# Kernel optimization log

Hardware: AMD Instinct MI355X
Metric: run time of the kernel (lower is better)

Reference implementation:

```python
import jax, jax.numpy as jnp
import numpy as np

B, D_IN, FD = 32768, 2048, 128
N1 = N2 = N3 = 4
T = 1.0  # temperature buffer value (eval mode)
LN_EPS = 1e-5

def _gelu(x):
    return jax.nn.gelu(x, approximate=False)  # torch nn.GELU default = exact erf

def setup_inputs() -> dict:
    key = jax.random.key(0)
    ks = iter(jax.random.split(key, 64))
    def rn(shape, s=0.02):
        return jax.random.normal(next(ks), shape, jnp.float32) * s
    inp = {"x": jax.random.normal(next(ks), (B, D_IN), jnp.float32)}
    # input_proj: Linear(2048,512) GELU Linear(512,256) LayerNorm(256)
    inp.update(ipW1=rn((D_IN, 512)), ipb1=jnp.zeros(512), ipW2=rn((512, 256)), ipb2=jnp.zeros(256),
               ln_g=jnp.ones(256), ln_b=jnp.zeros(256))
    def level(din, nc, pfx):
        return {pfx+"W3d": rn((din, 3)), pfx+"b3d": jnp.zeros(3),
                pfx+"c": rn((nc, 3), 0.3), pfx+"lr": jnp.zeros(nc),
                pfx+"f1W": rn((din, FD)), pfx+"f1b": jnp.zeros(FD),
                pfx+"f2W": rn((FD, FD)), pfx+"f2b": jnp.zeros(FD),
                pfx+"rW": rn((FD+3, nc)), pfx+"rb": jnp.zeros(nc)}
    inp.update(level(256, N1, "l1"))
    inp.update(level(FD, N2, "l2"))
    inp.update(level(FD, N3, "l3"))
    # expert_head: Linear(128+4+4+4, 256) GELU Linear(256, 64)
    inp.update(ehW1=rn((FD+N1+N2+N3, 256)), ehb1=jnp.zeros(256),
               ehW2=rn((256, N1*N2*N3)), ehb2=jnp.zeros(N1*N2*N3))
    return inp

def _level_fwd(x, W3d, b3d, c, f1W, f1b, f2W, f2b, rW, rb):
    # x: (B, din) -> probs (B, nc), features (B, FD)
    pos = x @ W3d + b3d                                   # (B, 3)
    d_sq = ((pos[:, None, :] - c[None, :, :]) ** 2).sum(-1)  # (B, nc)
    geo = -d_sq / (2.0 * T * T + 1e-8)                    # non-spectral geo signal
    feat = _gelu(x @ f1W + f1b) @ f2W + f2b               # (B, FD)
    logits = jnp.concatenate([feat, pos], axis=-1) @ rW + rb + 0.5 * geo
    probs = jax.nn.softmax(logits / max(T, 0.1), axis=-1)  # eval path: plain softmax
    return probs, feat

def _router_fwd(x, ipW1, ipb1, ipW2, ipb2, ln_g, ln_b,
                l1W3d, l1b3d, l1c, l1f1W, l1f1b, l1f2W, l1f2b, l1rW, l1rb,
                l2W3d, l2b3d, l2c, l2f1W, l2f1b, l2f2W, l2f2b, l2rW, l2rb,
                l3W3d, l3b3d, l3c, l3f1W, l3f1b, l3f2W, l3f2b, l3rW, l3rb,
                ehW1, ehb1, ehW2, ehb2):
    h = _gelu(x @ ipW1 + ipb1) @ ipW2 + ipb2
    mu = h.mean(-1, keepdims=True)
    var = ((h - mu) ** 2).mean(-1, keepdims=True)
    h = (h - mu) * jax.lax.rsqrt(var + LN_EPS) * ln_g + ln_b  # LayerNorm(256)
    p1, f1 = _level_fwd(h,  l1W3d, l1b3d, l1c, l1f1W, l1f1b, l1f2W, l1f2b, l1rW, l1rb)
    p2, f2 = _level_fwd(f1, l2W3d, l2b3d, l2c, l2f1W, l2f1b, l2f2W, l2f2b, l2rW, l2rb)
    p3, f3 = _level_fwd(f2, l3W3d, l3b3d, l3c, l3f1W, l3f1b, l3f2W, l3f2b, l3rW, l3rb)
    combined = jnp.concatenate([f3, p1, p2, p3], axis=-1)  # (B, 140)
    logits = _gelu(combined @ ehW1 + ehb1) @ ehW2 + ehb2   # (B, 64)
    expert_probs = jax.nn.softmax(logits / max(T, 0.1), axis=-1)
    return expert_probs

def reference(x, ipW1, ipb1, ipW2, ipb2, ln_g, ln_b,
              l1W3d, l1b3d, l1c, l1lr, l1f1W, l1f1b, l1f2W, l1f2b, l1rW, l1rb,
              l2W3d, l2b3d, l2c, l2lr, l2f1W, l2f1b, l2f2W, l2f2b, l2rW, l2rb,
              l3W3d, l3b3d, l3c, l3lr, l3f1W, l3f1b, l3f2W, l3f2b, l3rW, l3rb,
              ehW1, ehb1, ehW2, ehb2):
    # l?lr (log_radii) are unused in non-spectral mode, matching the source.
    expert_probs = _router_fwd(x, ipW1, ipb1, ipW2, ipb2, ln_g, ln_b,
                               l1W3d, l1b3d, l1c, l1f1W, l1f1b, l1f2W, l1f2b, l1rW, l1rb,
                               l2W3d, l2b3d, l2c, l2f1W, l2f1b, l2f2W, l2f2b, l2rW, l2rb,
                               l3W3d, l3b3d, l3c, l3f1W, l3f1b, l3f2W, l3f2b, l3rW, l3rb,
                               ehW1, ehb1, ehW2, ehb2)
    expert_ids = jnp.argmax(expert_probs, axis=-1)
    return expert_probs, expert_ids
```

## Files before the change

kernel.cpp:

```cpp
#include <hip/hip_runtime.h>
#include <hip/hip_bf16.h>
#include <cstdint>
#include <cstddef>


typedef short  s8v  __attribute__((ext_vector_type(8)));
typedef float  f4v  __attribute__((ext_vector_type(4)));
typedef float  f16v __attribute__((ext_vector_type(16)));
typedef unsigned int u32;

#define B_ROWS 32768

__device__ inline short f2bf(float x) {
    __hip_bfloat16 h = __float2bfloat16(x);
    return __builtin_bit_cast(short, h);
}
__device__ inline float bf2f(short s) {
    return __bfloat162float(__builtin_bit_cast(__hip_bfloat16, s));
}
__device__ inline float gelu_f(float x) {
    return 0.5f * x * (1.0f + erff(x * 0.70710678118654752440f));
}
__device__ inline void gload_lds16(const short* g, short* l) {
    __builtin_amdgcn_global_load_lds(
        (const __attribute__((address_space(1))) u32*)g,
        (__attribute__((address_space(3))) u32*)l, 16, 0, 0);
}

struct SplitDesc { const float* W; short* dst; int K, N, Kpad, blk0; };
struct SplitPack { SplitDesc d[10]; };

__global__ void split_all(SplitPack p) {
    const int bid = blockIdx.x;
    int i = 0;
    #pragma unroll
    for (int j = 1; j < 10; ++j) if (bid >= p.d[j].blk0) i = j;
    const SplitDesc& D = p.d[i];
    const int idx = (bid - D.blk0) * 256 + threadIdx.x;
    const int total = D.N * D.Kpad;
    if (idx >= total) return;
    const int n = idx / D.Kpad, k = idx - n * D.Kpad;
    const float v = (k < D.K) ? D.W[(size_t)k * D.N + n] : 0.0f;
    const short hs = f2bf(v);
    D.dst[idx] = hs;
    D.dst[total + idx] = f2bf(v - bf2f(hs));
}

template<int BM, int BN, int EPI>
__launch_bounds__(256, 2)
__global__ void gemm32(const float* __restrict__ A, int lda,
                       const short* __restrict__ Bsp, int ldb, int NK,
                       const float* __restrict__ bias, int K, int N, int ntiles,
                       float* __restrict__ out, float* __restrict__ out2)
{
    constexpr int MF  = BM / 64;
    constexpr int NFw = BN / 64;
    constexpr int BUF = (BM + BN) * 64;
    constexpr int FPT = BM / 8;
    constexpr int TPR = 32 / FPT;
    constexpr int nBI = BN / 32;
    __shared__ short smem[2 * BUF];

    const int tid = threadIdx.x;
    const int l   = tid & 63, wid = tid >> 6;
    const int wr  = wid >> 1, wc = wid & 1;
    const int bid = blockIdx.x;
    const int ntb = bid % ntiles, mtb = bid / ntiles;
    const int m0  = mtb * BM, n0 = ntb * BN;

    const int ar = tid / TPR, aseg = tid % TPR;
    const float* aP = A + (size_t)(m0 + ar) * lda + aseg * FPT;

    const short* bg[nBI];
    {
        const int cs = (l & 7) ^ (l >> 3);
        const int plane = cs >> 2, kslot = cs & 3;
        #pragma unroll
        for (int j = 0; j < nBI; ++j) {
            const int col = (wid * nBI + j) * 8 + (l >> 3);
            bg[j] = Bsp + (size_t)plane * NK + (size_t)(n0 + col) * ldb + kslot * 8;
        }
    }

    f16v acc[MF][NFw];
    #pragma unroll
    for (int m = 0; m < MF; ++m)
        #pragma unroll
        for (int n = 0; n < NFw; ++n) acc[m][n] = (f16v)0.0f;

    f4v areg[FPT / 4];

    auto loadA = [&](int t) {
        const float* p = aP + t * 32;
        #pragma unroll
        for (int i = 0; i < FPT / 4; ++i) areg[i] = *(const f4v*)(p + i * 4);
    };
    auto stageB = [&](int t, short* buf) {
        short* Bb = buf + BM * 64;
        #pragma unroll
        for (int j = 0; j < nBI; ++j)
            gload_lds16(bg[j] + t * 32, Bb + (wid * nBI + j) * 512);
    };
    auto writeA = [&](short* buf) {
        #pragma unroll
        for (int c = 0; c < FPT / 8; ++c) {
            s8v hi, lo;
            #pragma unroll
            for (int e = 0; e < 8; ++e) {
                const float v = areg[c * 2 + (e >> 2)][e & 3];
                const short hs = f2bf(v);
                hi[e] = hs; lo[e] = f2bf(v - bf2f(hs));
            }
            const int csh = aseg * (FPT / 8) + c;
            *(s8v*)&buf[ar * 64 + ((csh    ) ^ (ar & 7)) * 8] = hi;
            *(s8v*)&buf[ar * 64 + ((csh + 4) ^ (ar & 7)) * 8] = lo;
        }
    };
    auto compute = [&](const short* buf) {
        const short* Ab = buf;
        const short* Bb = buf + BM * 64;
        #pragma unroll
        for (int ks = 0; ks < 2; ++ks) {
            const int csb = ks * 2 + (l >> 5);
            s8v ah[MF], al[MF], bh[NFw], bl[NFw];
            #pragma unroll
            for (int m = 0; m < MF; ++m) {
                const int row = wr * (BM / 2) + m * 32 + (l & 31);
                ah[m] = *(const s8v*)&Ab[row * 64 + ((csb    ) ^ (row & 7)) * 8];
                al[m] = *(const s8v*)&Ab[row * 64 + ((csb + 4) ^ (row & 7)) * 8];
            }
            #pragma unroll
            for (int n = 0; n < NFw; ++n) {
                const int col = wc * (BN / 2) + n * 32 + (l & 31);
                bh[n] = *(const s8v*)&Bb[col * 64 + ((csb    ) ^ (col & 7)) * 8];
                bl[n] = *(const s8v*)&Bb[col * 64 + ((csb + 4) ^ (col & 7)) * 8];
            }
            __builtin_amdgcn_s_setprio(1);
            #pragma unroll
            for (int m = 0; m < MF; ++m)
                #pragma unroll
                for (int n = 0; n < NFw; ++n) {
                    acc[m][n] = __builtin_amdgcn_mfma_f32_32x32x16_bf16(ah[m], bh[n], acc[m][n], 0, 0, 0);
                    acc[m][n] = __builtin_amdgcn_mfma_f32_32x32x16_bf16(ah[m], bl[n], acc[m][n], 0, 0, 0);
                    acc[m][n] = __builtin_amdgcn_mfma_f32_32x32x16_bf16(al[m], bh[n], acc[m][n], 0, 0, 0);
                }
            __builtin_amdgcn_s_setprio(0);
        }
    };

    const int NT = K / 32;
    loadA(0);
    stageB(0, smem);
    writeA(smem);
    __syncthreads();
    for (int t = 0; t < NT; ++t) {
        short* curb = smem + (t & 1) * BUF;
        short* nxtb = smem + ((t & 1) ^ 1) * BUF;
        const bool pf = (t + 1 < NT);
        if (pf) { loadA(t + 1); stageB(t + 1, nxtb); }
        compute(curb);
        if (pf) writeA(nxtb);
        __syncthreads();
    }

    if constexpr (EPI <= 1) {
        #pragma unroll
        for (int m = 0; m < MF; ++m) {
            #pragma unroll
            for (int n = 0; n < NFw; ++n) {
                const int gcol = n0 + wc * (BN / 2) + n * 32 + (l & 31);
                const float bv = bias[gcol];
                #pragma unroll
                for (int r = 0; r < 16; ++r) {
                    const int grow = m0 + wr * (BM / 2) + m * 32
                                   + (r & 3) + 8 * (r >> 2) + 4 * (l >> 5);
                    float xv = acc[m][n][r] + bv;
                    if constexpr (EPI == 0) xv = gelu_f(xv);
                    out[(size_t)grow * N + gcol] = xv;
                }
            }
        }
    } else {
        float* LT = reinterpret_cast<float*>(smem);
        const int gcolL = wc * 32 + (l & 31);
        const float bv = bias[gcolL];
        #pragma unroll
        for (int r = 0; r < 16; ++r) {
            const int row = wr * 32 + (r & 3) + 8 * (r >> 2) + 4 * (l >> 5);
            LT[row * 64 + gcolL] = acc[0][0][r] + bv;
        }
        __syncthreads();
        const int r = tid >> 2, q = tid & 3;
        const float* Lr = LT + r * 64 + q * 16;
        float mx = Lr[0];
        #pragma unroll
        for (int c = 1; c < 16; ++c) mx = fmaxf(mx, Lr[c]);
        mx = fmaxf(mx, __shfl_xor(mx, 1));
        mx = fmaxf(mx, __shfl_xor(mx, 2));
        float ev[16]; float s = 0.0f;
        #pragma unroll
        for (int c = 0; c < 16; ++c) { ev[c] = expf(Lr[c] - mx); s += ev[c]; }
        s += __shfl_xor(s, 1);
        s += __shfl_xor(s, 2);
        float pmax = -1.0f; int arg = 0;
        #pragma unroll
        for (int c = 0; c < 16; ++c) {
            const float pv = ev[c] / s;
            out[(size_t)(m0 + r) * 64 + q * 16 + c] = pv;
            if (pv > pmax) { pmax = pv; arg = q * 16 + c; }
        }
        #pragma unroll
        for (int off = 1; off <= 2; off <<= 1) {
            const float po = __shfl_xor(pmax, off);
            const int   ao = __shfl_xor(arg, off);
            if (po > pmax || (po == pmax && ao < arg)) { pmax = po; arg = ao; }
        }
        if (q == 0) out2[m0 + r] = (float)arg;
    }
}

__global__ __launch_bounds__(256) void ln_kernel(float* __restrict__ H,
                                                 const float* __restrict__ G,
                                                 const float* __restrict__ Bv)
{
    const int row = blockIdx.x * 4 + (threadIdx.x >> 6);
    const int l   = threadIdx.x & 63;
    float* hr = H + (size_t)row * 256;
    f4v v = *reinterpret_cast<const f4v*>(&hr[l * 4]);
    float s = v[0] + v[1] + v[2] + v[3];
    #pragma unroll
    for (int o = 32; o; o >>= 1) s += __shfl_xor(s, o);
    const float mu = s * 0.00390625f;
    f4v d = v - mu;
    float q = d[0]*d[0] + d[1]*d[1] + d[2]*d[2] + d[3]*d[3];
    #pragma unroll
    for (int o = 32; o; o >>= 1) q += __shfl_xor(q, o);
    const float var = q * 0.00390625f;
    const float sc  = 1.0f / sqrtf(var + 1e-5f);
    f4v gg = *reinterpret_cast<const f4v*>(&G[l * 4]);
    f4v bb = *reinterpret_cast<const f4v*>(&Bv[l * 4]);
    f4v o4 = d * sc * gg + bb;
    *reinterpret_cast<f4v*>(&hr[l * 4]) = o4;
}

__global__ __launch_bounds__(256) void p_kernel(
    const float* __restrict__ X, int din,
    const float* __restrict__ F,
    const float* __restrict__ W3d, const float* __restrict__ b3d,
    const float* __restrict__ cc,
    const float* __restrict__ rW, const float* __restrict__ rb,
    float* __restrict__ P)
{
    const int row = blockIdx.x * 4 + (threadIdx.x >> 6);
    const int l   = threadIdx.x & 63;
    float px0 = 0.f, px1 = 0.f, px2 = 0.f;
    const int per = din >> 6;
    const float* xr = X + (size_t)row * din;
    for (int i = 0; i < per; ++i) {
        const int k = l + (i << 6);
        const float xv = xr[k];
        px0 += xv * W3d[k*3 + 0];
        px1 += xv * W3d[k*3 + 1];
        px2 += xv * W3d[k*3 + 2];
    }
    float g0 = 0.f, g1 = 0.f, g2 = 0.f, g3 = 0.f;
    const float* fr = F + (size_t)row * 128;
    #pragma unroll
    for (int i = 0; i < 2; ++i) {
        const int k = l + (i << 6);
        const float fv = fr[k];
        g0 += fv * rW[k*4 + 0]; g1 += fv * rW[k*4 + 1];
        g2 += fv * rW[k*4 + 2]; g3 += fv * rW[k*4 + 3];
    }
    #pragma unroll
    for (int o = 32; o; o >>= 1) {
        px0 += __shfl_xor(px0, o); px1 += __shfl_xor(px1, o); px2 += __shfl_xor(px2, o);
        g0  += __shfl_xor(g0, o);  g1  += __shfl_xor(g1, o);
        g2  += __shfl_xor(g2, o);  g3  += __shfl_xor(g3, o);
    }
    if (l == 0) {
        const float pos0 = px0 + b3d[0], pos1 = px1 + b3d[1], pos2 = px2 + b3d[2];
        float lg[4];
        float mx = -1e30f;
        float gg[4] = {g0, g1, g2, g3};
        #pragma unroll
        for (int c = 0; c < 4; ++c) {
            float a = gg[c] + rb[c]
                    + pos0 * rW[512 + c] + pos1 * rW[516 + c] + pos2 * rW[520 + c];
            const float d0 = pos0 - cc[c*3 + 0];
            const float d1 = pos1 - cc[c*3 + 1];
            const float d2 = pos2 - cc[c*3 + 2];
            a += 0.5f * (-(d0*d0 + d1*d1 + d2*d2) / 2.00000001f);
            lg[c] = a;
            mx = fmaxf(mx, a);
        }
        const float e0 = expf(lg[0]-mx), e1 = expf(lg[1]-mx),
                    e2 = expf(lg[2]-mx), e3 = expf(lg[3]-mx);
        const float s = e0 + e1 + e2 + e3;
        float* pr = P + (size_t)row * 4;
        pr[0] = e0/s; pr[1] = e1/s; pr[2] = e2/s; pr[3] = e3/s;
    }
}

__global__ void concat_kernel(const float* __restrict__ f3,
                              const float* __restrict__ P1,
                              const float* __restrict__ P2,
                              const float* __restrict__ P3,
                              float* __restrict__ C)
{
    const int idx = blockIdx.x * 256 + threadIdx.x;
    const int row = idx / 160, j = idx - row * 160;
    float v;
    if      (j < 128) v = f3[(size_t)row * 128 + j];
    else if (j < 132) v = P1[(size_t)row * 4 + (j - 128)];
    else if (j < 136) v = P2[(size_t)row * 4 + (j - 132)];
    else if (j < 140) v = P3[(size_t)row * 4 + (j - 136)];
    else              v = 0.0f;
    C[idx] = v;
}

extern "C" void kernel_launch(void* const* d_in, const int* in_sizes, int n_in,
                              void* d_out, int out_size, void* d_ws, size_t ws_size,
                              hipStream_t stream)
{
    (void)in_sizes; (void)n_in; (void)out_size; (void)ws_size;

    const float* x    = (const float*)d_in[0];
    const float* ipW1 = (const float*)d_in[1];
    const float* ipb1 = (const float*)d_in[2];
    const float* ipW2 = (const float*)d_in[3];
    const float* ipb2 = (const float*)d_in[4];
    const float* ln_g = (const float*)d_in[5];
    const float* ln_b = (const float*)d_in[6];
    const float* W3d[3] = {(const float*)d_in[7],  (const float*)d_in[17], (const float*)d_in[27]};
    const float* b3d[3] = {(const float*)d_in[8],  (const float*)d_in[18], (const float*)d_in[28]};
    const float* cc[3]  = {(const float*)d_in[9],  (const float*)d_in[19], (const float*)d_in[29]};
    const float* f1W[3] = {(const float*)d_in[11], (const float*)d_in[21], (const float*)d_in[31]};
    const float* f1b[3] = {(const float*)d_in[12], (const float*)d_in[22], (const float*)d_in[32]};
    const float* f2W[3] = {(const float*)d_in[13], (const float*)d_in[23], (const float*)d_in[33]};
    const float* f2b[3] = {(const float*)d_in[14], (const float*)d_in[24], (const float*)d_in[34]};
    const float* rW[3]  = {(const float*)d_in[15], (const float*)d_in[25], (const float*)d_in[35]};
    const float* rb[3]  = {(const float*)d_in[16], (const float*)d_in[26], (const float*)d_in[36]};
    const float* ehW1 = (const float*)d_in[37];
    const float* ehb1 = (const float*)d_in[38];
    const float* ehW2 = (const float*)d_in[39];
    const float* ehb2 = (const float*)d_in[40];

    size_t off = 0;
    auto take = [&](size_t bytes) -> void* {
        void* p = (char*)d_ws + off;
        off += (bytes + 255) & ~(size_t)255;
        return p;
    };
    auto takeW = [&](int N, int Kpad) -> short* {
        return (short*)take((size_t)2 * N * Kpad * 2);
    };
    short* W1s = takeW(512, 2048);
    short* W2s = takeW(256, 512);
    short* L1a = takeW(128, 256);
    short* L1b = takeW(128, 128);
    short* L2a = takeW(128, 128);
    short* L2b = takeW(128, 128);
    short* L3a = takeW(128, 128);
    short* L3b = takeW(128, 128);
    short* E1s = takeW(256, 160);
    short* E2s = takeW(64, 256);
    float* h1 = (float*)take((size_t)B_ROWS * 512 * 4);
    float* h2 = (float*)take((size_t)B_ROWS * 256 * 4);
    float* zg = (float*)take((size_t)B_ROWS * 128 * 4);
    float* f1 = (float*)take((size_t)B_ROWS * 128 * 4);
    float* f2 = (float*)take((size_t)B_ROWS * 128 * 4);
    float* f3 = (float*)take((size_t)B_ROWS * 128 * 4);
    float* p1 = (float*)take((size_t)B_ROWS * 4 * 4);
    float* p2 = (float*)take((size_t)B_ROWS * 4 * 4);
    float* p3 = (float*)take((size_t)B_ROWS * 4 * 4);
    float* comb = h1;
    float* geh  = (float*)((char*)h1 + ((size_t)22 << 20));

    SplitPack sp;
    int blk = 0;
    auto desc = [&](int i, const float* W, short* dst, int K, int N, int Kpad) {
        sp.d[i] = {W, dst, K, N, Kpad, blk};
        blk += (N * Kpad + 255) / 256;
    };
    desc(0, ipW1,   W1s, 2048, 512, 2048);
    desc(1, ipW2,   W2s,  512, 256,  512);
    desc(2, f1W[0], L1a,  256, 128,  256);
    desc(3, f2W[0], L1b,  128, 128,  128);
    desc(4, f1W[1], L2a,  128, 128,  128);
    desc(5, f2W[1], L2b,  128, 128,  128);
    desc(6, f1W[2], L3a,  128, 128,  128);
    desc(7, f2W[2], L3b,  128, 128,  128);
    desc(8, ehW1,   E1s,  140, 256,  160);
    desc(9, ehW2,   E2s,  256,  64,  256);
    split_all<<<blk, 256, 0, stream>>>(sp);

    const dim3 blkT(256);
    constexpr int MG128 = B_ROWS / 128;
    constexpr int MG64  = B_ROWS / 64;

    gemm32<128,128,0><<<MG128*4, blkT, 0, stream>>>(x,  2048, W1s, 2048, 512*2048, ipb1, 2048, 512, 4, h1, nullptr);
    gemm32<128,128,1><<<MG128*2, blkT, 0, stream>>>(h1,  512, W2s,  512, 256*512,  ipb2,  512, 256, 2, h2, nullptr);
    ln_kernel<<<B_ROWS/4, 256, 0, stream>>>(h2, ln_g, ln_b);

    gemm32<64,128,0><<<MG64, blkT, 0, stream>>>(h2, 256, L1a, 256, 128*256, f1b[0], 256, 128, 1, zg, nullptr);
    gemm32<64,128,1><<<MG64, blkT, 0, stream>>>(zg, 128, L1b, 128, 128*128, f2b[0], 128, 128, 1, f1, nullptr);
    p_kernel<<<B_ROWS/4, 256, 0, stream>>>(h2, 256, f1, W3d[0], b3d[0], cc[0], rW[0], rb[0], p1);

    gemm32<64,128,0><<<MG64, blkT, 0, stream>>>(f1, 128, L2a, 128, 128*128, f1b[1], 128, 128, 1, zg, nullptr);
    gemm32<64,128,1><<<MG64, blkT, 0, stream>>>(zg, 128, L2b, 128, 128*128, f2b[1], 128, 128, 1, f2, nullptr);
    p_kernel<<<B_ROWS/4, 256, 0, stream>>>(f1, 128, f2, W3d[1], b3d[1], cc[1], rW[1], rb[1], p2);

    gemm32<64,128,0><<<MG64, blkT, 0, stream>>>(f2, 128, L3a, 128, 128*128, f1b[2], 128, 128, 1, zg, nullptr);
    gemm32<64,128,1><<<MG64, blkT, 0, stream>>>(zg, 128, L3b, 128, 128*128, f2b[2], 128, 128, 1, f3, nullptr);
    p_kernel<<<B_ROWS/4, 256, 0, stream>>>(f2, 128, f3, W3d[2], b3d[2], cc[2], rW[2], rb[2], p3);

    concat_kernel<<<(B_ROWS*160)/256, 256, 0, stream>>>(f3, p1, p2, p3, comb);
    gemm32<64,128,0><<<MG64*2, blkT, 0, stream>>>(comb, 160, E1s, 160, 256*160, ehb1, 160, 256, 2, geh, nullptr);
    gemm32<64,64,2><<<MG64, blkT, 0, stream>>>(geh, 256, E2s, 256, 64*256, ehb2, 256, 64, 1,
                                               (float*)d_out, (float*)d_out + (size_t)B_ROWS * 64);
}
```

Baseline: 533.2 us.

## Add specialized first-layer GEMM with pre-swizzled split-bf16 weight image

Replaces the generic gemm32 for the 2048->512 input projection with a dedicated kernel. It reads the fp32 activations directly and splits them into bf16 hi/lo planes in registers. The weights are pre-split into a swizzled tile image that can be loaded straight into LDS with global_load_lds, and the block-to-tile mapping is XCD-aware. Single-stage LDS with register prefetch of the next A tile aims to cut conversion and layout overhead, but adds a new weight-prep kernel and a fixed-shape path that only fits these dimensions.

```diff
diff --git a/kernel.cpp b/kernel.cpp
--- a/kernel.cpp
+++ b/kernel.cpp
@@ -27,14 +27,150 @@
         (__attribute__((address_space(3))) u32*)l, 16, 0, 0);
 }
 
+__global__ void split_w1_img(const float* __restrict__ W, short* __restrict__ img)
+{
+    const int idx = blockIdx.x * 256 + threadIdx.x;
+    const int p = idx & 7;
+    const int n = (idx >> 3) & 511;
+    const int t = idx >> 12;
+    const int cs = p ^ (n & 7);
+    const int plane = cs >> 2, kc = cs & 3;
+    const int kbase = t * 32 + kc * 8;
+    s8v v8;
+    #pragma unroll
+    for (int e = 0; e < 8; ++e) {
+        const float v = W[(size_t)(kbase + e) * 512 + n];
+        const short h = f2bf(v);
+        v8[e] = plane ? f2bf(v - bf2f(h)) : h;
+    }
+    *(s8v*)&img[(size_t)((t * 512 + n) * 64 + p * 8)] = v8;
+}
+
+__launch_bounds__(256, 4)
+__global__ void gemm1k(const float* __restrict__ X,
+                       const short* __restrict__ Bimg,
+                       const float* __restrict__ bias,
+                       float* __restrict__ out)
+{
+    __shared__ short smem[128 * 64 * 2];
+    short* Ab = smem;
+    short* Bb = smem + 128 * 64;
+
+    const int tid = threadIdx.x;
+    const int l = tid & 63, wid = tid >> 6;
+    const int wr = wid >> 1, wc = wid & 1;
+
+    const int d = blockIdx.x;
+    const int xcd = d & 7;
+    const int m0 = ((xcd & 1) * 128 + (d >> 3)) * 128;
+    const int n0 = (xcd >> 1) * 128;
+
+    const int ar = tid & 127, ah = tid >> 7;
+    const float* xP = X + (size_t)(m0 + ar) * 2048 + ah * 16;
+    short* awr = Ab + ar * 64;
+    const int pw0 = ((ah * 2    ) ^ (ar & 7)) * 8;
+    const int pw1 = ((ah * 2 + 1) ^ (ar & 7)) * 8;
+    const int pw2 = ((ah * 2 + 4) ^ (ar & 7)) * 8;
+    const int pw3 = ((ah * 2 + 5) ^ (ar & 7)) * 8;
+
+    const short* bP = Bimg + (size_t)n0 * 64 + (size_t)(wid * 4) * 512 + (size_t)l * 8;
+    short* bD = Bb + wid * 4 * 512;
+
+    f16v acc[2][2];
+    #pragma unroll
+    for (int m = 0; m < 2; ++m)
+        #pragma unroll
+        for (int n = 0; n < 2; ++n) acc[m][n] = (f16v)0.0f;
+
+    f4v cur0, cur1, cur2, cur3;
+    cur0 = *(const f4v*)(xP + 0);
+    cur1 = *(const f4v*)(xP + 4);
+    cur2 = *(const f4v*)(xP + 8);
+    cur3 = *(const f4v*)(xP + 12);
+
+    for (int t = 0; t < 64; ++t) {
+        s8v hi0, hi1, lo0, lo1;
+        #pragma unroll
+        for (int e = 0; e < 4; ++e) {
+            float v;
+            short h;
+            v = cur0[e]; h = f2bf(v); hi0[e]     = h; lo0[e]     = f2bf(v - bf2f(h));
+            v = cur1[e]; h = f2bf(v); hi0[e + 4] = h; lo0[e + 4] = f2bf(v - bf2f(h));
+            v = cur2[e]; h = f2bf(v); hi1[e]     = h; lo1[e]     = f2bf(v - bf2f(h));
+            v = cur3[e]; h = f2bf(v); hi1[e + 4] = h; lo1[e + 4] = f2bf(v - bf2f(h));
+        }
+        __syncthreads();
+        *(s8v*)&awr[pw0] = hi0;
+        *(s8v*)&awr[pw1] = hi1;
+        *(s8v*)&awr[pw2] = lo0;
+        *(s8v*)&awr[pw3] = lo1;
+        {
+            const short* bt = bP + (size_t)t * 32768;
+            gload_lds16(bt,          bD);
+            gload_lds16(bt +  512,   bD + 512);
+            gload_lds16(bt + 1024,   bD + 1024);
+            gload_lds16(bt + 1536,   bD + 1536);
+        }
+        if (t < 63) {
+            const float* p = xP + (t + 1) * 32;
+            cur0 = *(const f4v*)(p + 0);
+            cur1 = *(const f4v*)(p + 4);
+            cur2 = *(const f4v*)(p + 8);
+            cur3 = *(const f4v*)(p + 12);
+        }
+        __syncthreads();
+
+        #pragma unroll
+        for (int ks = 0; ks < 2; ++ks) {
+            const int ph = (ks * 2 + (l >> 5)) ^ (l & 7);
+            s8v ahf[2], alf[2], bhf[2], blf[2];
+            #pragma unroll
+            for (int m = 0; m < 2; ++m) {
+                const int row = wr * 64 + m * 32 + (l & 31);
+                ahf[m] = *(const s8v*)&Ab[row * 64 + ph * 8];
+                alf[m] = *(const s8v*)&Ab[row * 64 + (ph ^ 4) * 8];
+            }
+            #pragma unroll
+            for (int n = 0; n < 2; ++n) {
+                const int col = wc * 64 + n * 32 + (l & 31);
+                bhf[n] = *(const s8v*)&Bb[col * 64 + ph * 8];
+                blf[n] = *(const s8v*)&Bb[col * 64 + (ph ^ 4) * 8];
+            }
+            #pragma unroll
+            for (int m = 0; m < 2; ++m)
+                #pragma unroll
+                for (int n = 0; n < 2; ++n) {
+                    acc[m][n] = __builtin_amdgcn_mfma_f32_32x32x16_bf16(ahf[m], bhf[n], acc[m][n], 0, 0, 0);
+                    acc[m][n] = __builtin_amdgcn_mfma_f32_32x32x16_bf16(ahf[m], blf[n], acc[m][n], 0, 0, 0);
+                    acc[m][n] = __builtin_amdgcn_mfma_f32_32x32x16_bf16(alf[m], bhf[n], acc[m][n], 0, 0, 0);
+                }
+        }
+    }
+
+    #pragma unroll
+    for (int m = 0; m < 2; ++m) {
+        #pragma unroll
+        for (int n = 0; n < 2; ++n) {
+            const int gcol = n0 + wc * 64 + n * 32 + (l & 31);
+            const float bv = bias[gcol];
+            #pragma unroll
+            for (int r = 0; r < 16; ++r) {
+                const int grow = m0 + wr * 64 + m * 32
+                               + (r & 3) + 8 * (r >> 2) + 4 * (l >> 5);
+                out[(size_t)grow * 512 + gcol] = gelu_f(acc[m][n][r] + bv);
+            }
+        }
+    }
+}
+
 struct SplitDesc { const float* W; short* dst; int K, N, Kpad, blk0; };
-struct SplitPack { SplitDesc d[10]; };
+struct SplitPack { SplitDesc d[9]; };
 
 __global__ void split_all(SplitPack p) {
     const int bid = blockIdx.x;
     int i = 0;
     #pragma unroll
-    for (int j = 1; j < 10; ++j) if (bid >= p.d[j].blk0) i = j;
+    for (int j = 1; j < 9; ++j) if (bid >= p.d[j].blk0) i = j;
     const SplitDesc& D = p.d[i];
     const int idx = (bid - D.blk0) * 256 + threadIdx.x;
     const int total = D.N * D.Kpad;
@@ -355,7 +491,7 @@
     auto takeW = [&](int N, int Kpad) -> short* {
         return (short*)take((size_t)2 * N * Kpad * 2);
     };
-    short* W1s = takeW(512, 2048);
+    short* W1img = (short*)take((size_t)64 * 512 * 64 * 2);
     short* W2s = takeW(256, 512);
     short* L1a = takeW(128, 256);
     short* L1b = takeW(128, 128);
@@ -377,29 +513,29 @@
     float* comb = h1;
     float* geh  = (float*)((char*)h1 + ((size_t)22 << 20));
 
+    split_w1_img<<<(64 * 512 * 8) / 256, 256, 0, stream>>>(ipW1, W1img);
     SplitPack sp;
     int blk = 0;
     auto desc = [&](int i, const float* W, short* dst, int K, int N, int Kpad) {
         sp.d[i] = {W, dst, K, N, Kpad, blk};
         blk += (N * Kpad + 255) / 256;
     };
-    desc(0, ipW1,   W1s, 2048, 512, 2048);
-    desc(1, ipW2,   W2s,  512, 256,  512);
-    desc(2, f1W[0], L1a,  256, 128,  256);
-    desc(3, f2W[0], L1b,  128, 128,  128);
-    desc(4, f1W[1], L2a,  128, 128,  128);
-    desc(5, f2W[1], L2b,  128, 128,  128);
-    desc(6, f1W[2], L3a,  128, 128,  128);
-    desc(7, f2W[2], L3b,  128, 128,  128);
-    desc(8, ehW1,   E1s,  140, 256,  160);
-    desc(9, ehW2,   E2s,  256,  64,  256);
+    desc(0, ipW2,   W2s,  512, 256,  512);
+    desc(1, f1W[0], L1a,  256, 128,  256);
+    desc(2, f2W[0], L1b,  128, 128,  128);
+    desc(3, f1W[1], L2a,  128, 128,  128);
+    desc(4, f2W[1], L2b,  128, 128,  128);
+    desc(5, f1W[2], L3a,  128, 128,  128);
+    desc(6, f2W[2], L3b,  128, 128,  128);
+    desc(7, ehW1,   E1s,  140, 256,  160);
+    desc(8, ehW2,   E2s,  256,  64,  256);
     split_all<<<blk, 256, 0, stream>>>(sp);
 
     const dim3 blkT(256);
     constexpr int MG128 = B_ROWS / 128;
     constexpr int MG64  = B_ROWS / 64;
 
-    gemm32<128,128,0><<<MG128*4, blkT, 0, stream>>>(x,  2048, W1s, 2048, 512*2048, ipb1, 2048, 512, 4, h1, nullptr);
+    gemm1k<<<1024, blkT, 0, stream>>>(x, W1img, ipb1, h1);
     gemm32<128,128,1><<<MG128*2, blkT, 0, stream>>>(h1,  512, W2s,  512, 256*512,  ipb2,  512, 256, 2, h2, nullptr);
     ln_kernel<<<B_ROWS/4, 256, 0, stream>>>(h2, ln_g, ln_b);
 
```

New measurement: 495.0 us. 1.08x faster.
